# Performance work log

Measured on AMD Instinct MI355X. Metric: run time of the kernel, lower is better.

The kernel has to match this reference:

```python
import jax, jax.numpy as jnp
import numpy as np

B, T, V, E, H, O = 512, 64, 1024, 256, 512, 256


def setup_inputs() -> dict:
    key = jax.random.key(0)
    ks = jax.random.split(key, 9)
    s = 0.02
    return {
        "message": jax.random.normal(ks[0], (B, T, V), jnp.float32),
        "W_emb": jax.random.normal(ks[1], (E, V), jnp.float32) * s,   # Linear(vocab, embed).weight
        "b_emb": jnp.zeros((E,), jnp.float32),
        "W_ih": jax.random.normal(ks[2], (4 * H, E), jnp.float32) * s,  # LSTMCell weight_ih (i,f,g,o)
        "b_ih": jnp.zeros((4 * H,), jnp.float32),
        "W_hh": jax.random.normal(ks[3], (4 * H, H), jnp.float32) * s,  # LSTMCell weight_hh
        "b_hh": jnp.zeros((4 * H,), jnp.float32),
        "W_agent": jax.random.normal(ks[4], (O, H), jnp.float32) * s,   # agent Linear(hidden, out)
        "b_agent": jnp.zeros((O,), jnp.float32),
    }


def reference(message, W_emb, b_emb, W_ih, b_ih, W_hh, b_hh, W_agent, b_agent):
    # Embedding for all timesteps at once: [B,T,V] @ [E,V]^T -> [B,T,E]
    emb = jnp.einsum('btv,ev->bte', message, W_emb) + b_emb
    # Precompute input-side gate preactivations for every step: [B,T,4H]
    x_gates = jnp.einsum('bte,ge->btg', emb, W_ih) + (b_ih + b_hh)
    x_gates = jnp.swapaxes(x_gates, 0, 1)  # [T,B,4H] for scan
    Bsz = message.shape[0]
    Hh = W_hh.shape[1]

    def step(carry, xg):
        h, c = carry
        g = xg + h @ W_hh.T                      # [B,4H]
        i, f, gg, o = jnp.split(g, 4, axis=-1)   # PyTorch LSTMCell gate order i,f,g,o
        i = jax.nn.sigmoid(i)
        f = jax.nn.sigmoid(f)
        gg = jnp.tanh(gg)
        o = jax.nn.sigmoid(o)
        c = f * c + i * gg
        h = o * jnp.tanh(c)
        return (h, c), h

    h0 = jnp.zeros((Bsz, Hh), message.dtype)
    _, hs = jax.lax.scan(step, (h0, h0), x_gates)  # hs: [T,B,H]
    # Agent head applied to every step's hidden state, output [B,T,O]
    out = jnp.einsum('tbh,oh->bto', hs, W_agent) + b_agent
    return out
```

## Files before the change

### kernel.cpp

```cpp
#include <hip/hip_runtime.h>

typedef unsigned short u16;
typedef unsigned int u32;
typedef __attribute__((ext_vector_type(8))) short bf16x8;
typedef __attribute__((ext_vector_type(4))) float f32x4;

__device__ inline u16 f2bf(float x) {
  u32 u = __float_as_uint(x);
  u32 r = (u + 0x7FFFu + ((u >> 16) & 1u)) >> 16;
  return (u16)r;
}
__device__ inline float bf2f(u16 h) { return __uint_as_float(((u32)h) << 16); }
__device__ inline float sigm(float x) { return 1.f / (1.f + __expf(-x)); }
__device__ inline float tanh_s(float x) {
  float ax = fabsf(x);
  float e = __expf(2.f * ax);
  float t = 1.f - 2.f / (e + 1.f);
  return copysignf(t, x);
}

__global__ void cvt_f32_bf16(const float* __restrict__ s, u16* __restrict__ d, int n) {
  int i = (blockIdx.x * 256 + threadIdx.x) * 4;
  if (i < n) {
    float4 f = *(const float4*)&s[i];
    u32 lo = (u32)f2bf(f.x) | ((u32)f2bf(f.y) << 16);
    u32 hi = (u32)f2bf(f.z) | ((u32)f2bf(f.w) << 16);
    uint2 v; v.x = lo; v.y = hi;
    *(uint2*)&d[i] = v;
  }
}

__global__ void bias_add(const float* __restrict__ a, const float* __restrict__ b,
                         float* __restrict__ d, int n) {
  int i = blockIdx.x * 256 + threadIdx.x;
  if (i < n) d[i] = a[i] + b[i];
}

template <int A_F32, int OUT_BF16>
__global__ __launch_bounds__(256) void gemm_bt(
    const void* __restrict__ Ap, const u16* __restrict__ Bp,
    const float* __restrict__ bias, void* __restrict__ Cp,
    int K, int lda, int ldb, int ldc) {
  __shared__ u16 Alds[128 * 64];
  __shared__ u16 Blds[128 * 64];
  const int tid = threadIdx.x;
  const int lane = tid & 63;
  const int w = tid >> 6;
  const int wm = w >> 1, wn = w & 1;
  const int m0 = blockIdx.x * 128, n0 = blockIdx.y * 128;
  const int r = lane & 15, kb = lane >> 4;

  f32x4 acc[4][4];
#pragma unroll
  for (int m = 0; m < 4; ++m)
#pragma unroll
    for (int n = 0; n < 4; ++n) acc[m][n] = (f32x4)0.f;

  for (int k0 = 0; k0 < K; k0 += 64) {
#pragma unroll
    for (int p = 0; p < 4; ++p) {
      int ch = p * 256 + tid;
      int row = ch >> 3;
      int col = (ch & 7) * 8;
      if (A_F32) {
        const float* s = (const float*)Ap + (size_t)(m0 + row) * lda + k0 + col;
        float4 f0 = *(const float4*)s;
        float4 f1 = *(const float4*)(s + 4);
        uint4 v;
        v.x = (u32)f2bf(f0.x) | ((u32)f2bf(f0.y) << 16);
        v.y = (u32)f2bf(f0.z) | ((u32)f2bf(f0.w) << 16);
        v.z = (u32)f2bf(f1.x) | ((u32)f2bf(f1.y) << 16);
        v.w = (u32)f2bf(f1.z) | ((u32)f2bf(f1.w) << 16);
        *(uint4*)&Alds[row * 64 + col] = v;
      } else {
        uint4 v = *(const uint4*)((const u16*)Ap + (size_t)(m0 + row) * lda + k0 + col);
        *(uint4*)&Alds[row * 64 + col] = v;
      }
      uint4 vb = *(const uint4*)(Bp + (size_t)(n0 + row) * ldb + k0 + col);
      *(uint4*)&Blds[row * 64 + col] = vb;
    }
    __syncthreads();
#pragma unroll
    for (int ks = 0; ks < 2; ++ks) {
      int kk = ks * 32 + kb * 8;
      bf16x8 af[4], bfr[4];
#pragma unroll
      for (int m = 0; m < 4; ++m)
        af[m] = *(const bf16x8*)&Alds[(wm * 64 + m * 16 + r) * 64 + kk];
#pragma unroll
      for (int n = 0; n < 4; ++n)
        bfr[n] = *(const bf16x8*)&Blds[(wn * 64 + n * 16 + r) * 64 + kk];
#pragma unroll
      for (int m = 0; m < 4; ++m)
#pragma unroll
        for (int n = 0; n < 4; ++n)
          acc[m][n] = __builtin_amdgcn_mfma_f32_16x16x32_bf16(af[m], bfr[n], acc[m][n], 0, 0, 0);
    }
    __syncthreads();
  }

  const int r4 = kb * 4;
#pragma unroll
  for (int m = 0; m < 4; ++m) {
#pragma unroll
    for (int n = 0; n < 4; ++n) {
      int row = m0 + wm * 64 + m * 16 + r4;
      int col = n0 + wn * 64 + n * 16 + (lane & 15);
      float bv = bias[col];
#pragma unroll
      for (int j = 0; j < 4; ++j) {
        float v = acc[m][n][j] + bv;
        if (OUT_BF16)
          ((u16*)Cp)[(size_t)(row + j) * ldc + col] = f2bf(v);
        else
          ((float*)Cp)[(size_t)(row + j) * ldc + col] = v;
      }
    }
  }
}

__global__ __launch_bounds__(256) void lstm_step(
    const u16* __restrict__ xg,
    const u16* __restrict__ Whh,
    const u16* __restrict__ hs_r,
    u16* __restrict__ hs_w,
    float* __restrict__ cst,
    int t) {
  __shared__ u16 Ah[32 * 64];
  __shared__ u16 Bw[128 * 64];
  __shared__ float G[4 * 1024];
  const int tid = threadIdx.x;
  const int lane = tid & 63;
  const int g = tid >> 6;
  const int b0 = blockIdx.x * 32, hc0 = blockIdx.y * 32;
  const int r = lane & 15, kb = lane >> 4;

  f32x4 acc[2][2];
#pragma unroll
  for (int m = 0; m < 2; ++m)
#pragma unroll
    for (int n = 0; n < 2; ++n) acc[m][n] = (f32x4)0.f;

  if (t > 0) {
    for (int k0 = 0; k0 < 512; k0 += 64) {
      {
        int row = tid >> 3;
        int col = (tid & 7) * 8;
        uint4 v = *(const uint4*)&hs_r[((size_t)(b0 + row) * 64 + (t - 1)) * 512 + k0 + col];
        *(uint4*)&Ah[row * 64 + col] = v;
      }
#pragma unroll
      for (int p = 0; p < 4; ++p) {
        int ch = p * 256 + tid;
        int row = ch >> 3;
        int col = (ch & 7) * 8;
        int gg = row >> 5, rr = row & 31;
        uint4 v = *(const uint4*)&Whh[((size_t)gg * 512 + hc0 + rr) * 512 + k0 + col];
        *(uint4*)&Bw[row * 64 + col] = v;
      }
      __syncthreads();
#pragma unroll
      for (int ks = 0; ks < 2; ++ks) {
        int kk = ks * 32 + kb * 8;
        bf16x8 af[2], bfr[2];
#pragma unroll
        for (int m = 0; m < 2; ++m)
          af[m] = *(const bf16x8*)&Ah[(m * 16 + r) * 64 + kk];
#pragma unroll
        for (int n = 0; n < 2; ++n)
          bfr[n] = *(const bf16x8*)&Bw[(g * 32 + n * 16 + r) * 64 + kk];
#pragma unroll
        for (int m = 0; m < 2; ++m)
#pragma unroll
          for (int n = 0; n < 2; ++n)
            acc[m][n] = __builtin_amdgcn_mfma_f32_16x16x32_bf16(af[m], bfr[n], acc[m][n], 0, 0, 0);
      }
      __syncthreads();
    }
  }

#pragma unroll
  for (int m = 0; m < 2; ++m)
#pragma unroll
    for (int n = 0; n < 2; ++n)
#pragma unroll
      for (int j = 0; j < 4; ++j)
        G[g * 1024 + ((m * 2 + n) * 4 + j) * 64 + lane] = acc[m][n][j];
  __syncthreads();

#pragma unroll
  for (int q = 0; q < 4; ++q) {
    int e = q * 256 + tid;
    int l = e & 63;
    int rr = e >> 6;
    int j = rr & 3;
    int mn = rr >> 2;
    int m = mn >> 1, n = mn & 1;
    int brow = m * 16 + (l >> 4) * 4 + j;
    int col = n * 16 + (l & 15);
    int b = b0 + brow;
    int hcol = hc0 + col;
    size_t xrow = ((size_t)b * 64 + t) * 2048;
    float vi = G[0 * 1024 + e] + bf2f(xg[xrow + 0 * 512 + hcol]);
    float vf = G[1 * 1024 + e] + bf2f(xg[xrow + 1 * 512 + hcol]);
    float vg = G[2 * 1024 + e] + bf2f(xg[xrow + 2 * 512 + hcol]);
    float vo = G[3 * 1024 + e] + bf2f(xg[xrow + 3 * 512 + hcol]);
    float ii = sigm(vi);
    float ff = sigm(vf);
    float gg = tanh_s(vg);
    float oo = sigm(vo);
    float cp = (t == 0) ? 0.f : cst[(size_t)b * 512 + hcol];
    float cn = ff * cp + ii * gg;
    float hn = oo * tanh_s(cn);
    cst[(size_t)b * 512 + hcol] = cn;
    hs_w[((size_t)b * 64 + t) * 512 + hcol] = f2bf(hn);
  }
}

extern "C" void kernel_launch(void* const* d_in, const int* in_sizes, int n_in,
                              void* d_out, int out_size, void* d_ws, size_t ws_size,
                              hipStream_t stream) {
  (void)in_sizes; (void)n_in; (void)out_size; (void)ws_size;
  const float* msg   = (const float*)d_in[0];
  const float* W_emb = (const float*)d_in[1];
  const float* b_emb = (const float*)d_in[2];
  const float* W_ih  = (const float*)d_in[3];
  const float* b_ih  = (const float*)d_in[4];
  const float* W_hh  = (const float*)d_in[5];
  const float* b_hh  = (const float*)d_in[6];
  const float* W_ag  = (const float*)d_in[7];
  const float* b_ag  = (const float*)d_in[8];
  float* out = (float*)d_out;

  char* p = (char*)d_ws;
  u16* Wemb_b = (u16*)p;  p += (size_t)256 * 1024 * 2;
  u16* Wih_b  = (u16*)p;  p += (size_t)2048 * 256 * 2;
  u16* Whh_b  = (u16*)p;  p += (size_t)2048 * 512 * 2;
  u16* Wag_b  = (u16*)p;  p += (size_t)256 * 512 * 2;
  float* bc   = (float*)p; p += (size_t)2048 * 4;
  p = (char*)(((size_t)p + 255) & ~(size_t)255);
  u16* emb_b = (u16*)p;   p += (size_t)32768 * 256 * 2;
  u16* xg    = (u16*)p;   p += (size_t)32768 * 2048 * 2;
  u16* hs    = (u16*)p;   p += (size_t)32768 * 512 * 2;
  float* cst = (float*)p;

  cvt_f32_bf16<<<256, 256, 0, stream>>>(W_emb, Wemb_b, 256 * 1024);
  cvt_f32_bf16<<<512, 256, 0, stream>>>(W_ih, Wih_b, 2048 * 256);
  cvt_f32_bf16<<<1024, 256, 0, stream>>>(W_hh, Whh_b, 2048 * 512);
  cvt_f32_bf16<<<128, 256, 0, stream>>>(W_ag, Wag_b, 256 * 512);
  bias_add<<<8, 256, 0, stream>>>(b_ih, b_hh, bc, 2048);

  gemm_bt<1, 1><<<dim3(256, 2), 256, 0, stream>>>(msg, Wemb_b, b_emb, emb_b,
                                                  1024, 1024, 1024, 256);
  gemm_bt<0, 1><<<dim3(256, 16), 256, 0, stream>>>(emb_b, Wih_b, bc, xg,
                                                   256, 256, 256, 2048);
  for (int t = 0; t < 64; ++t)
    lstm_step<<<dim3(16, 16), 256, 0, stream>>>(xg, Whh_b, hs, hs, cst, t);
  gemm_bt<0, 0><<<dim3(256, 2), 256, 0, stream>>>(hs, Wag_b, b_ag, out,
                                                  512, 512, 512, 256);
}
```

Baseline: 917.0 us.

## Replace per-timestep LSTM launches with persistent kernel and swizzle GEMM LDS

```diff
diff --git a/kernel.cpp b/kernel.cpp
--- a/kernel.cpp
+++ b/kernel.cpp
@@ -34,6 +34,11 @@
                          float* __restrict__ d, int n) {
   int i = blockIdx.x * 256 + threadIdx.x;
   if (i < n) d[i] = a[i] + b[i];
+}
+
+__global__ void zero_u32(u32* __restrict__ p, int n) {
+  int i = blockIdx.x * 256 + threadIdx.x;
+  if (i < n) p[i] = 0;
 }
 
 template <int A_F32, int OUT_BF16>
@@ -62,6 +67,7 @@
       int ch = p * 256 + tid;
       int row = ch >> 3;
       int col = (ch & 7) * 8;
+      int scol = col ^ ((row & 7) << 3);
       if (A_F32) {
         const float* s = (const float*)Ap + (size_t)(m0 + row) * lda + k0 + col;
         float4 f0 = *(const float4*)s;
@@ -71,13 +77,13 @@
         v.y = (u32)f2bf(f0.z) | ((u32)f2bf(f0.w) << 16);
         v.z = (u32)f2bf(f1.x) | ((u32)f2bf(f1.y) << 16);
         v.w = (u32)f2bf(f1.z) | ((u32)f2bf(f1.w) << 16);
-        *(uint4*)&Alds[row * 64 + col] = v;
+        *(uint4*)&Alds[row * 64 + scol] = v;
       } else {
         uint4 v = *(const uint4*)((const u16*)Ap + (size_t)(m0 + row) * lda + k0 + col);
-        *(uint4*)&Alds[row * 64 + col] = v;
+        *(uint4*)&Alds[row * 64 + scol] = v;
       }
       uint4 vb = *(const uint4*)(Bp + (size_t)(n0 + row) * ldb + k0 + col);
-      *(uint4*)&Blds[row * 64 + col] = vb;
+      *(uint4*)&Blds[row * 64 + scol] = vb;
     }
     __syncthreads();
 #pragma unroll
@@ -85,11 +91,15 @@
       int kk = ks * 32 + kb * 8;
       bf16x8 af[4], bfr[4];
 #pragma unroll
-      for (int m = 0; m < 4; ++m)
-        af[m] = *(const bf16x8*)&Alds[(wm * 64 + m * 16 + r) * 64 + kk];
-#pragma unroll
-      for (int n = 0; n < 4; ++n)
-        bfr[n] = *(const bf16x8*)&Blds[(wn * 64 + n * 16 + r) * 64 + kk];
+      for (int m = 0; m < 4; ++m) {
+        int row = wm * 64 + m * 16 + r;
+        af[m] = *(const bf16x8*)&Alds[row * 64 + (kk ^ ((row & 7) << 3))];
+      }
+#pragma unroll
+      for (int n = 0; n < 4; ++n) {
+        int row = wn * 64 + n * 16 + r;
+        bfr[n] = *(const bf16x8*)&Blds[row * 64 + (kk ^ ((row & 7) << 3))];
+      }
 #pragma unroll
       for (int m = 0; m < 4; ++m)
 #pragma unroll
@@ -119,101 +129,84 @@
   }
 }
 
-__global__ __launch_bounds__(256) void lstm_step(
+__global__ __launch_bounds__(256, 1) void lstm_persist(
     const u16* __restrict__ xg,
     const u16* __restrict__ Whh,
-    const u16* __restrict__ hs_r,
-    u16* __restrict__ hs_w,
-    float* __restrict__ cst,
-    int t) {
-  __shared__ u16 Ah[32 * 64];
-  __shared__ u16 Bw[128 * 64];
-  __shared__ float G[4 * 1024];
+    u16* __restrict__ h2,
+    u16* __restrict__ hs,
+    u32* ctr) {
   const int tid = threadIdx.x;
   const int lane = tid & 63;
-  const int g = tid >> 6;
-  const int b0 = blockIdx.x * 32, hc0 = blockIdx.y * 32;
-  const int r = lane & 15, kb = lane >> 4;
-
-  f32x4 acc[2][2];
-#pragma unroll
-  for (int m = 0; m < 2; ++m)
-#pragma unroll
-    for (int n = 0; n < 2; ++n) acc[m][n] = (f32x4)0.f;
-
-  if (t > 0) {
-    for (int k0 = 0; k0 < 512; k0 += 64) {
-      {
-        int row = tid >> 3;
-        int col = (tid & 7) * 8;
-        uint4 v = *(const uint4*)&hs_r[((size_t)(b0 + row) * 64 + (t - 1)) * 512 + k0 + col];
-        *(uint4*)&Ah[row * 64 + col] = v;
-      }
-#pragma unroll
-      for (int p = 0; p < 4; ++p) {
-        int ch = p * 256 + tid;
-        int row = ch >> 3;
-        int col = (ch & 7) * 8;
-        int gg = row >> 5, rr = row & 31;
-        uint4 v = *(const uint4*)&Whh[((size_t)gg * 512 + hc0 + rr) * 512 + k0 + col];
-        *(uint4*)&Bw[row * 64 + col] = v;
-      }
+  const int w = tid >> 6;
+  const int g = blockIdx.x & 7;
+  const int m = blockIdx.x >> 3;
+  const int b0 = g * 64;
+  const int hc0 = m * 16;
+  const int col = lane & 15;
+  const int q = lane >> 4;
+
+  bf16x8 Breg[4][16];
+#pragma unroll
+  for (int n = 0; n < 4; ++n)
+#pragma unroll
+    for (int kf = 0; kf < 16; ++kf)
+      Breg[n][kf] = *(const bf16x8*)&Whh[((size_t)(n * 512 + hc0 + col)) * 512 + kf * 32 + q * 8];
+
+  float cst[4] = {0.f, 0.f, 0.f, 0.f};
+  const int arow = b0 + w * 16 + col;
+  const int gr0 = b0 + w * 16 + q * 4;
+
+  for (int t = 0; t < 64; ++t) {
+    float xv[4][4];
+#pragma unroll
+    for (int j = 0; j < 4; ++j) {
+      const u16* xp = xg + ((size_t)(gr0 + j) * 64 + t) * 2048 + hc0 + col;
+#pragma unroll
+      for (int n = 0; n < 4; ++n) xv[n][j] = bf2f(xp[n * 512]);
+    }
+
+    f32x4 acc[4];
+#pragma unroll
+    for (int n = 0; n < 4; ++n) acc[n] = (f32x4)0.f;
+
+    if (t > 0) {
+      const u16* hp = h2 + (size_t)((t - 1) & 1) * (512 * 512) + (size_t)arow * 512;
+#pragma unroll
+      for (int kf = 0; kf < 16; ++kf) {
+        bf16x8 a = *(const bf16x8*)&hp[kf * 32 + q * 8];
+#pragma unroll
+        for (int n = 0; n < 4; ++n)
+          acc[n] = __builtin_amdgcn_mfma_f32_16x16x32_bf16(a, Breg[n][kf], acc[n], 0, 0, 0);
+      }
+    }
+
+    u16* hw = h2 + (size_t)(t & 1) * (512 * 512);
+#pragma unroll
+    for (int j = 0; j < 4; ++j) {
+      float vi = acc[0][j] + xv[0][j];
+      float vf = acc[1][j] + xv[1][j];
+      float vg = acc[2][j] + xv[2][j];
+      float vo = acc[3][j] + xv[3][j];
+      float ii = sigm(vi), ff = sigm(vf), gg = tanh_s(vg), oo = sigm(vo);
+      float cn = ff * cst[j] + ii * gg;
+      cst[j] = cn;
+      u16 hb = f2bf(oo * tanh_s(cn));
+      int br = gr0 + j;
+      hw[(size_t)br * 512 + hc0 + col] = hb;
+      hs[((size_t)br * 64 + t) * 512 + hc0 + col] = hb;
+    }
+
+    if (t < 63) {
+      __threadfence();
       __syncthreads();
-#pragma unroll
-      for (int ks = 0; ks < 2; ++ks) {
-        int kk = ks * 32 + kb * 8;
-        bf16x8 af[2], bfr[2];
-#pragma unroll
-        for (int m = 0; m < 2; ++m)
-          af[m] = *(const bf16x8*)&Ah[(m * 16 + r) * 64 + kk];
-#pragma unroll
-        for (int n = 0; n < 2; ++n)
-          bfr[n] = *(const bf16x8*)&Bw[(g * 32 + n * 16 + r) * 64 + kk];
-#pragma unroll
-        for (int m = 0; m < 2; ++m)
-#pragma unroll
-          for (int n = 0; n < 2; ++n)
-            acc[m][n] = __builtin_amdgcn_mfma_f32_16x16x32_bf16(af[m], bfr[n], acc[m][n], 0, 0, 0);
+      if (tid == 0) {
+        __hip_atomic_fetch_add(&ctr[t * 8 + g], 1u, __ATOMIC_ACQ_REL, __HIP_MEMORY_SCOPE_AGENT);
+        while (__hip_atomic_load(&ctr[t * 8 + g], __ATOMIC_ACQUIRE, __HIP_MEMORY_SCOPE_AGENT) < 32u)
+          __builtin_amdgcn_s_sleep(4);
       }
       __syncthreads();
-    }
-  }
-
-#pragma unroll
-  for (int m = 0; m < 2; ++m)
-#pragma unroll
-    for (int n = 0; n < 2; ++n)
-#pragma unroll
-      for (int j = 0; j < 4; ++j)
-        G[g * 1024 + ((m * 2 + n) * 4 + j) * 64 + lane] = acc[m][n][j];
-  __syncthreads();
-
-#pragma unroll
-  for (int q = 0; q < 4; ++q) {
-    int e = q * 256 + tid;
-    int l = e & 63;
-    int rr = e >> 6;
-    int j = rr & 3;
-    int mn = rr >> 2;
-    int m = mn >> 1, n = mn & 1;
-    int brow = m * 16 + (l >> 4) * 4 + j;
-    int col = n * 16 + (l & 15);
-    int b = b0 + brow;
-    int hcol = hc0 + col;
-    size_t xrow = ((size_t)b * 64 + t) * 2048;
-    float vi = G[0 * 1024 + e] + bf2f(xg[xrow + 0 * 512 + hcol]);
-    float vf = G[1 * 1024 + e] + bf2f(xg[xrow + 1 * 512 + hcol]);
-    float vg = G[2 * 1024 + e] + bf2f(xg[xrow + 2 * 512 + hcol]);
-    float vo = G[3 * 1024 + e] + bf2f(xg[xrow + 3 * 512 + hcol]);
-    float ii = sigm(vi);
-    float ff = sigm(vf);
-    float gg = tanh_s(vg);
-    float oo = sigm(vo);
-    float cp = (t == 0) ? 0.f : cst[(size_t)b * 512 + hcol];
-    float cn = ff * cp + ii * gg;
-    float hn = oo * tanh_s(cn);
-    cst[(size_t)b * 512 + hcol] = cn;
-    hs_w[((size_t)b * 64 + t) * 512 + hcol] = f2bf(hn);
+      __threadfence();
+    }
   }
 }
 
@@ -242,20 +235,21 @@
   u16* emb_b = (u16*)p;   p += (size_t)32768 * 256 * 2;
   u16* xg    = (u16*)p;   p += (size_t)32768 * 2048 * 2;
   u16* hs    = (u16*)p;   p += (size_t)32768 * 512 * 2;
-  float* cst = (float*)p;
+  u16* h2    = (u16*)p;   p += (size_t)2 * 512 * 512 * 2;
+  u32* ctr   = (u32*)p;   p += (size_t)64 * 8 * 4;
 
   cvt_f32_bf16<<<256, 256, 0, stream>>>(W_emb, Wemb_b, 256 * 1024);
   cvt_f32_bf16<<<512, 256, 0, stream>>>(W_ih, Wih_b, 2048 * 256);
   cvt_f32_bf16<<<1024, 256, 0, stream>>>(W_hh, Whh_b, 2048 * 512);
   cvt_f32_bf16<<<128, 256, 0, stream>>>(W_ag, Wag_b, 256 * 512);
   bias_add<<<8, 256, 0, stream>>>(b_ih, b_hh, bc, 2048);
+  zero_u32<<<2, 256, 0, stream>>>(ctr, 64 * 8);
 
   gemm_bt<1, 1><<<dim3(256, 2), 256, 0, stream>>>(msg, Wemb_b, b_emb, emb_b,
                                                   1024, 1024, 1024, 256);
   gemm_bt<0, 1><<<dim3(256, 16), 256, 0, stream>>>(emb_b, Wih_b, bc, xg,
                                                    256, 256, 256, 2048);
-  for (int t = 0; t < 64; ++t)
-    lstm_step<<<dim3(16, 16), 256, 0, stream>>>(xg, Whh_b, hs, hs, cst, t);
+  lstm_persist<<<256, 256, 0, stream>>>(xg, Whh_b, h2, hs, ctr);
   gemm_bt<0, 0><<<dim3(256, 2), 256, 0, stream>>>(hs, Wag_b, b_ag, out,
                                                   512, 512, 512, 256);
 }
```

New measurement: 3.560 ms. 3.88x slower.
